# Optimization experiments

Hardware: AMD Instinct MI355X
Metric: run time of the kernel (lower is better)

## Reference

```python
import jax, jax.numpy as jnp
import numpy as np

N = 65536      # tokens
D = 512        # input_dim
H = 8          # num_heads
HD = 64        # head_dim
FF = 2048      # hidden_dim
EPS = 1e-5


def _layer_norm(x, g, b):
    mu = jnp.mean(x, axis=-1, keepdims=True)
    var = jnp.mean(jnp.square(x - mu), axis=-1, keepdims=True)
    return (x - mu) * jax.lax.rsqrt(var + EPS) * g + b


def setup_inputs() -> dict:
    key = jax.random.key(0)
    ks = jax.random.split(key, 12)
    s_d = 1.0 / np.sqrt(D)
    s_f = 1.0 / np.sqrt(FF)
    return {
        "x":   jax.random.normal(ks[0], (N, D), jnp.float32),
        # Linear weights stored [in, out] (transpose of torch's [out, in])
        "Wq":  jax.random.uniform(ks[1], (D, D), jnp.float32, -s_d, s_d),
        "bq":  jnp.zeros((D,), jnp.float32),
        "Wk":  jax.random.uniform(ks[2], (D, D), jnp.float32, -s_d, s_d),
        "bk":  jnp.zeros((D,), jnp.float32),
        "Wv":  jax.random.uniform(ks[3], (D, D), jnp.float32, -s_d, s_d),
        "bv":  jnp.zeros((D,), jnp.float32),
        "ln1_g": jnp.ones((D,), jnp.float32),
        "ln1_b": jnp.zeros((D,), jnp.float32),
        "W1":  jax.random.uniform(ks[4], (D, FF), jnp.float32, -s_d, s_d),
        "b1":  jnp.zeros((FF,), jnp.float32),
        "W2":  jax.random.uniform(ks[5], (FF, D), jnp.float32, -s_f, s_f),
        "b2":  jnp.zeros((D,), jnp.float32),
        "ln2_g": jnp.ones((D,), jnp.float32),
        "ln2_b": jnp.zeros((D,), jnp.float32),
    }


def reference(x, Wq, bq, Wk, bk, Wv, bv, ln1_g, ln1_b, W1, b1, W2, b2, ln2_g, ln2_b):
    n = x.shape[0]
    # --- multi-head attention (per-token head mixing, as in source) ---
    q = (x @ Wq + bq).reshape(n, H, HD)
    k = (x @ Wk + bk).reshape(n, H, HD)
    v = (x @ Wv + bv).reshape(n, H, HD)
    # score[n] = q[n] @ k[n]^T : [H, H] per token
    score = jnp.einsum("nhd,ngd->nhg", q, k) / jnp.sqrt(jnp.float32(HD))
    attn = jax.nn.softmax(score, axis=-1)
    ctx = jnp.einsum("nhg,ngd->nhd", attn, v).reshape(n, D)
    y = _layer_norm(x + ctx, ln1_g, ln1_b)
    # --- feed forward with residual + layer norm ---
    h = jax.nn.relu(y @ W1 + b1)
    z = h @ W2 + b2 + y
    return _layer_norm(z, ln2_g, ln2_b)
```

## Files before the change

### kernel.cpp

```cpp
#include <hip/hip_runtime.h>
#include <cstdint>


typedef __attribute__((ext_vector_type(8))) short bf16x8;
typedef __attribute__((ext_vector_type(4))) float f32x4;
typedef __attribute__((ext_vector_type(8))) unsigned short u16x8;

__device__ __forceinline__ float bf2f(unsigned short u) {
  union { unsigned int i; float f; } v; v.i = ((unsigned int)u) << 16; return v.f;
}
__device__ __forceinline__ unsigned short f2bf(float f) {
  union { float f; unsigned int i; } v; v.f = f;
  unsigned int r = v.i + 0x7FFFu + ((v.i >> 16) & 1u);
  return (unsigned short)(r >> 16);
}

#define GLD16(g, l)                                                         \
  __builtin_amdgcn_global_load_lds(                                         \
      (const __attribute__((address_space(1))) void*)(g),                   \
      (__attribute__((address_space(3))) void*)(l), 16, 0, 0)

__global__ __launch_bounds__(256) void cast_f32_bf16(
    const float* __restrict__ in, ushort* __restrict__ out) {
  const size_t i = (size_t)blockIdx.x * 256 + threadIdx.x;
  const float4* p = (const float4*)in + i * 2;
  float4 a = p[0], b = p[1];
  u16x8 r;
  r[0] = f2bf(a.x); r[1] = f2bf(a.y); r[2] = f2bf(a.z); r[3] = f2bf(a.w);
  r[4] = f2bf(b.x); r[5] = f2bf(b.y); r[6] = f2bf(b.z); r[7] = f2bf(b.w);
  ((u16x8*)out)[i] = r;
}

__global__ __launch_bounds__(256) void transpose_cast(
    const float* __restrict__ W, ushort* __restrict__ Wt,
    int K, int Nn, int rowoff, int ldt) {
  __shared__ float tile[32][33];
  const int tx = threadIdx.x & 31, ty = threadIdx.x >> 5;
  const int nb = blockIdx.x * 32, kb = blockIdx.y * 32;
#pragma unroll
  for (int s = 0; s < 4; ++s)
    tile[ty + 8 * s][tx] = W[(size_t)(kb + ty + 8 * s) * Nn + nb + tx];
  __syncthreads();
#pragma unroll
  for (int s = 0; s < 4; ++s)
    Wt[(size_t)(rowoff + nb + ty + 8 * s) * ldt + kb + tx] =
        f2bf(tile[tx][ty + 8 * s]);
}

template <int EPI>
__global__ __launch_bounds__(512, 2) void gemm_bt(
    const ushort* __restrict__ A, const ushort* __restrict__ Bt,
    int N, int K, void* __restrict__ Cout,
    const float* __restrict__ bias0, const float* __restrict__ bias1,
    const float* __restrict__ bias2, const ushort* __restrict__ resid) {
  constexpr int BK = 32;
  __shared__ __align__(16) ushort lds[4 * 16384];
  const int tid = threadIdx.x;
  const int wid = tid >> 6, lane = tid & 63;
  const int wm = wid >> 2, wn = wid & 3;

  const int gx = gridDim.x;
  const int nwg = gx * gridDim.y;
  const int orig = blockIdx.y * gx + blockIdx.x;
  const int q8 = nwg >> 3, r8 = nwg & 7;
  const int xcd = orig & 7, loc = orig >> 3;
  const int swz = (xcd < r8) ? (xcd * (q8 + 1) + loc)
                             : (r8 * (q8 + 1) + (xcd - r8) * q8 + loc);
  const size_t m0 = (size_t)(swz / gx) * 256;
  const size_t n0 = (size_t)(swz % gx) * 256;
  const int NT = K / BK;

  const int sgcol = (((tid & 3) - ((tid >> 3) & 3)) & 3) << 3;
  const ushort* a0 = A + (m0 + (tid >> 2)) * (size_t)K + sgcol;
  const ushort* b0 = Bt + (n0 + (tid >> 2)) * (size_t)K + sgcol;
  const size_t rowK = 128 * (size_t)K;
  ushort* ldst = &lds[tid * 8];

#define STAGE_SLOT(t, sl)                                                   \
  {                                                                         \
    ushort* d = ldst + ((t) & 3) * 16384 + (sl) * 4096;                     \
    const ushort* g = (((sl) < 2) ? a0 : b0) + (size_t)(t) * BK +           \
                      (((sl) & 1) ? rowK : 0);                              \
    GLD16(g, d);                                                            \
  }

  const int cswz = ((((lane >> 4) + ((lane >> 1) & 3)) & 3) << 3);
  const int arow = wm * 128 + (lane & 15);
  const int brow = wn * 64 + (lane & 15);

  f32x4 acc[8][4] = {};

#pragma unroll
  for (int pt = 0; pt < 3; ++pt) {
    STAGE_SLOT(pt, 0); STAGE_SLOT(pt, 1);
    STAGE_SLOT(pt, 2); STAGE_SLOT(pt, 3);
  }

  for (int t = 0; t < NT; ++t) {
    if (t < NT - 2) {
      asm volatile("s_waitcnt vmcnt(8)" ::: "memory");
    } else if (t == NT - 2) {
      asm volatile("s_waitcnt vmcnt(4)" ::: "memory");
    } else {
      asm volatile("s_waitcnt vmcnt(0)" ::: "memory");
    }
    __builtin_amdgcn_s_barrier();

    const ushort* lA = &lds[(t & 3) * 16384];
    const ushort* lB = lA + 8192;

    if (t + 3 < NT) {
      STAGE_SLOT(t + 3, 0); STAGE_SLOT(t + 3, 1);
      STAGE_SLOT(t + 3, 2); STAGE_SLOT(t + 3, 3);
    }

    bf16x8 bfr[4], af[8];
#pragma unroll
    for (int ni = 0; ni < 4; ++ni)
      bfr[ni] = *(const bf16x8*)&lB[(brow + ni * 16) * 32 + cswz];
#pragma unroll
    for (int mi = 0; mi < 8; ++mi)
      af[mi] = *(const bf16x8*)&lA[(arow + mi * 16) * 32 + cswz];

    __builtin_amdgcn_s_setprio(1);
#pragma unroll
    for (int mi = 0; mi < 8; ++mi)
#pragma unroll
      for (int ni = 0; ni < 4; ++ni)
        acc[mi][ni] = __builtin_amdgcn_mfma_f32_16x16x32_bf16(
            af[mi], bfr[ni], acc[mi][ni], 0, 0, 0);
    __builtin_amdgcn_s_setprio(0);
  }
#undef STAGE_SLOT

  const int lm = lane & 15, lq = lane >> 4;
  size_t col[4];
  float bv[4];
#pragma unroll
  for (int ni = 0; ni < 4; ++ni) {
    col[ni] = n0 + wn * 64 + ni * 16 + lm;
    if (EPI == 0) {
      const float* bp = (n0 < 512) ? bias0 : ((n0 < 1024) ? bias1 : bias2);
      bv[ni] = bp[col[ni] & 511];
    } else {
      bv[ni] = bias0[col[ni]];
    }
  }
#pragma unroll
  for (int mi = 0; mi < 8; ++mi) {
#pragma unroll
    for (int j = 0; j < 4; ++j) {
      const size_t row = m0 + wm * 128 + mi * 16 + lq * 4 + j;
#pragma unroll
      for (int ni = 0; ni < 4; ++ni) {
        float v = acc[mi][ni][j] + bv[ni];
        if (EPI == 0) {
          ((ushort*)Cout)[row * N + col[ni]] = f2bf(v);
        } else if (EPI == 1) {
          ((ushort*)Cout)[row * N + col[ni]] = f2bf(fmaxf(v, 0.f));
        } else {
          v += bf2f(resid[row * N + col[ni]]);
          ((ushort*)Cout)[row * N + col[ni]] = f2bf(v);
        }
      }
    }
  }
}

__global__ __launch_bounds__(256) void attn_ln1(
    const ushort* __restrict__ qkv, const ushort* __restrict__ xb,
    const float* __restrict__ g1, const float* __restrict__ b1,
    ushort* __restrict__ y) {
  const int lane = threadIdx.x & 63;
  const size_t t = (size_t)blockIdx.x * 4 + (threadIdx.x >> 6);
  const ushort* base = qkv + t * 1536;
  float qd[8], kd[8], vd[8];
#pragma unroll
  for (int h = 0; h < 8; ++h) {
    qd[h] = bf2f(base[h * 64 + lane]);
    kd[h] = bf2f(base[512 + h * 64 + lane]);
    vd[h] = bf2f(base[1024 + h * 64 + lane]);
  }

  const bool lb0 = lane & 1, lb1 = lane & 2, lb2 = lane & 4;
  const bool lb3 = lane & 8, lb4 = lane & 16, lb5 = lane & 32;

  float c1[32];
#pragma unroll
  for (int f = 0; f < 32; ++f) {
    const int i0 = 2 * f, i1 = 2 * f + 1;
    const float a0 = qd[i0 >> 3] * kd[i0 & 7];
    const float a1 = qd[i1 >> 3] * kd[i1 & 7];
    const float keep = lb0 ? a1 : a0;
    const float send = lb0 ? a0 : a1;
    c1[f] = keep + __shfl_xor(send, 1, 64);
  }
  float c2[16];
#pragma unroll
  for (int f = 0; f < 16; ++f) {
    const float keep = lb1 ? c1[2 * f + 1] : c1[2 * f];
    const float send = lb1 ? c1[2 * f] : c1[2 * f + 1];
    c2[f] = keep + __shfl_xor(send, 2, 64);
  }
  float c3[8];
#pragma unroll
  for (int f = 0; f < 8; ++f) {
    const float keep = lb2 ? c2[2 * f + 1] : c2[2 * f];
    const float send = lb2 ? c2[2 * f] : c2[2 * f + 1];
    c3[f] = keep + __shfl_xor(send, 4, 64);
  }
  float c4[4];
#pragma unroll
  for (int f = 0; f < 4; ++f) {
    const float keep = lb3 ? c3[2 * f + 1] : c3[2 * f];
    const float send = lb3 ? c3[2 * f] : c3[2 * f + 1];
    c4[f] = keep + __shfl_xor(send, 8, 64);
  }
  float c5[2];
#pragma unroll
  for (int f = 0; f < 2; ++f) {
    const float keep = lb4 ? c4[2 * f + 1] : c4[2 * f];
    const float send = lb4 ? c4[2 * f] : c4[2 * f + 1];
    c5[f] = keep + __shfl_xor(send, 16, 64);
  }
  const float keep = lb5 ? c5[1] : c5[0];
  const float send = lb5 ? c5[0] : c5[1];
  const float s = keep + __shfl_xor(send, 32, 64);

  float mx = s;
  mx = fmaxf(mx, __shfl_xor(mx, 1, 64));
  mx = fmaxf(mx, __shfl_xor(mx, 2, 64));
  mx = fmaxf(mx, __shfl_xor(mx, 4, 64));
  const float e = __expf((s - mx) * 0.125f);
  float sum = e;
  sum += __shfl_xor(sum, 1, 64);
  sum += __shfl_xor(sum, 2, 64);
  sum += __shfl_xor(sum, 4, 64);
  const float a = e * __builtin_amdgcn_rcpf(sum);

  const int ai = __float_as_int(a);
  float r[8];
#pragma unroll
  for (int h = 0; h < 8; ++h) {
    float c = 0.f;
#pragma unroll
    for (int g = 0; g < 8; ++g) {
      const float w = __int_as_float(__builtin_amdgcn_readlane(ai, h * 8 + g));
      c = fmaf(w, vd[g], c);
    }
    r[h] = bf2f(xb[t * 512 + h * 64 + lane]) + c;
  }

  float sm = 0.f, sq = 0.f;
#pragma unroll
  for (int h = 0; h < 8; ++h) { sm += r[h]; sq += r[h] * r[h]; }
#pragma unroll
  for (int m = 1; m < 64; m <<= 1) {
    sm += __shfl_xor(sm, m, 64);
    sq += __shfl_xor(sq, m, 64);
  }
  const float mu = sm * (1.f / 512.f);
  const float var = sq * (1.f / 512.f) - mu * mu;
  const float rs = rsqrtf(var + 1e-5f);
#pragma unroll
  for (int h = 0; h < 8; ++h) {
    const int d = h * 64 + lane;
    y[t * 512 + d] = f2bf((r[h] - mu) * rs * g1[d] + b1[d]);
  }
}

__global__ __launch_bounds__(256) void ln_out(
    const ushort* __restrict__ zb, const float* __restrict__ g2,
    const float* __restrict__ b2, float* __restrict__ out) {
  const int lane = threadIdx.x & 63;
  const size_t t = (size_t)blockIdx.x * 4 + (threadIdx.x >> 6);
  const u16x8 v = ((const u16x8*)(zb + t * 512))[lane];
  float r[8];
  float sm = 0.f, sq = 0.f;
#pragma unroll
  for (int j = 0; j < 8; ++j) {
    r[j] = bf2f(v[j]);
    sm += r[j];
    sq += r[j] * r[j];
  }
#pragma unroll
  for (int m = 1; m < 64; m <<= 1) {
    sm += __shfl_xor(sm, m, 64);
    sq += __shfl_xor(sq, m, 64);
  }
  const float mu = sm * (1.f / 512.f);
  const float rs = rsqrtf(sq * (1.f / 512.f) - mu * mu + 1e-5f);
  const int d0 = lane * 8;
  const float4 ga = *(const float4*)(g2 + d0);
  const float4 gb = *(const float4*)(g2 + d0 + 4);
  const float4 ba = *(const float4*)(b2 + d0);
  const float4 bb = *(const float4*)(b2 + d0 + 4);
  float4 oa, ob;
  oa.x = (r[0] - mu) * rs * ga.x + ba.x;
  oa.y = (r[1] - mu) * rs * ga.y + ba.y;
  oa.z = (r[2] - mu) * rs * ga.z + ba.z;
  oa.w = (r[3] - mu) * rs * ga.w + ba.w;
  ob.x = (r[4] - mu) * rs * gb.x + bb.x;
  ob.y = (r[5] - mu) * rs * gb.y + bb.y;
  ob.z = (r[6] - mu) * rs * gb.z + bb.z;
  ob.w = (r[7] - mu) * rs * gb.w + bb.w;
  float* o = out + t * 512 + d0;
  *(float4*)o = oa;
  *(float4*)(o + 4) = ob;
}

extern "C" void kernel_launch(void* const* d_in, const int* in_sizes, int n_in,
                              void* d_out, int out_size, void* d_ws,
                              size_t ws_size, hipStream_t stream) {
  const float* x    = (const float*)d_in[0];
  const float* Wq   = (const float*)d_in[1];
  const float* bq   = (const float*)d_in[2];
  const float* Wk   = (const float*)d_in[3];
  const float* bk   = (const float*)d_in[4];
  const float* Wv   = (const float*)d_in[5];
  const float* bv   = (const float*)d_in[6];
  const float* ln1g = (const float*)d_in[7];
  const float* ln1b = (const float*)d_in[8];
  const float* W1   = (const float*)d_in[9];
  const float* b1   = (const float*)d_in[10];
  const float* W2   = (const float*)d_in[11];
  const float* b2   = (const float*)d_in[12];
  const float* ln2g = (const float*)d_in[13];
  const float* ln2b = (const float*)d_in[14];
  float* out = (float*)d_out;

  const int Ntok = in_sizes[0] / 512;

  char* ws = (char*)d_ws;
  ushort* Wqkvt = (ushort*)ws;
  ushort* W1t   = Wqkvt + (size_t)1536 * 512;
  ushort* W2t   = W1t + (size_t)2048 * 512;
  const size_t woff = ((size_t)1536 * 512 + (size_t)2048 * 512 +
                       (size_t)512 * 2048) * 2;

  size_t avail = (ws_size > woff) ? (ws_size - woff) : 0;
  long long Cll = (long long)(avail / 9216);
  Cll = (Cll / 256) * 256;
  if (Cll > 32768) Cll = 32768;
  if (Cll > Ntok) Cll = Ntok;
  if (Cll < 256) Cll = 256;
  const int C = (int)Cll;

  char* cb = ws + woff;
  ushort* xb  = (ushort*)cb;
  ushort* y   = xb + (size_t)C * 512;
  ushort* qkv = y + (size_t)C * 512;
  ushort* hb  = qkv + (size_t)C * 1536;
  ushort* zb  = qkv;

  transpose_cast<<<dim3(16, 16), dim3(256), 0, stream>>>(Wq, Wqkvt, 512, 512, 0, 512);
  transpose_cast<<<dim3(16, 16), dim3(256), 0, stream>>>(Wk, Wqkvt, 512, 512, 512, 512);
  transpose_cast<<<dim3(16, 16), dim3(256), 0, stream>>>(Wv, Wqkvt, 512, 512, 1024, 512);
  transpose_cast<<<dim3(64, 16), dim3(256), 0, stream>>>(W1, W1t, 512, 2048, 0, 512);
  transpose_cast<<<dim3(16, 64), dim3(256), 0, stream>>>(W2, W2t, 2048, 512, 0, 2048);

  for (int t0 = 0; t0 < Ntok; t0 += C) {
    const int Cc = (Ntok - t0 < C) ? (Ntok - t0) : C;
    const float* xc = x + (size_t)t0 * 512;

    cast_f32_bf16<<<dim3((Cc * 512) / 2048), dim3(256), 0, stream>>>(xc, xb);

    gemm_bt<0><<<dim3(1536 / 256, Cc / 256), dim3(512), 0, stream>>>(
        xb, Wqkvt, 1536, 512, qkv, bq, bk, bv, nullptr);

    attn_ln1<<<dim3(Cc / 4), dim3(256), 0, stream>>>(qkv, xb, ln1g, ln1b, y);

    gemm_bt<1><<<dim3(2048 / 256, Cc / 256), dim3(512), 0, stream>>>(
        y, W1t, 2048, 512, hb, b1, nullptr, nullptr, nullptr);

    gemm_bt<2><<<dim3(512 / 256, Cc / 256), dim3(512), 0, stream>>>(
        hb, W2t, 512, 2048, zb, b2, nullptr, nullptr, y);

    ln_out<<<dim3(Cc / 4), dim3(256), 0, stream>>>(
        zb, ln2g, ln2b, out + (size_t)t0 * 512);
  }
}
```

Baseline: 637.1 us.

## Restructure GEMM mainloop into BK=64 double-buffered, four-phase interleaved schedule

```diff
diff --git a/kernel.cpp b/kernel.cpp
--- a/kernel.cpp
+++ b/kernel.cpp
@@ -48,16 +48,17 @@
 }
 
 template <int EPI>
-__global__ __launch_bounds__(512, 2) void gemm_bt(
+__global__ __launch_bounds__(512, 1) void gemm_bt(
     const ushort* __restrict__ A, const ushort* __restrict__ Bt,
     int N, int K, void* __restrict__ Cout,
     const float* __restrict__ bias0, const float* __restrict__ bias1,
     const float* __restrict__ bias2, const ushort* __restrict__ resid) {
-  constexpr int BK = 32;
-  __shared__ __align__(16) ushort lds[4 * 16384];
+  __shared__ __align__(16) ushort lds[2 * 32768];
   const int tid = threadIdx.x;
   const int wid = tid >> 6, lane = tid & 63;
   const int wm = wid >> 2, wn = wid & 3;
+  const int li = lane & 15, q = lane >> 4;
+  const int sw = (lane >> 1) & 7;
 
   const int gx = gridDim.x;
   const int nwg = gx * gridDim.y;
@@ -68,77 +69,136 @@
                              : (r8 * (q8 + 1) + (xcd - r8) * q8 + loc);
   const size_t m0 = (size_t)(swz / gx) * 256;
   const size_t n0 = (size_t)(swz % gx) * 256;
-  const int NT = K / BK;
-
-  const int sgcol = (((tid & 3) - ((tid >> 3) & 3)) & 3) << 3;
-  const ushort* a0 = A + (m0 + (tid >> 2)) * (size_t)K + sgcol;
-  const ushort* b0 = Bt + (n0 + (tid >> 2)) * (size_t)K + sgcol;
-  const size_t rowK = 128 * (size_t)K;
-  ushort* ldst = &lds[tid * 8];
-
-#define STAGE_SLOT(t, sl)                                                   \
+  const int NT = K >> 6;
+
+  const int ssrc = (((tid & 7) - ((tid >> 4) & 7)) & 7) << 3;
+  const ushort* asrc = A + (m0 + (tid >> 3)) * (size_t)K + ssrc;
+  const ushort* bsrc = Bt + (n0 + (tid >> 3)) * (size_t)K + ssrc;
+  const size_t rowK64 = 64 * (size_t)K;
+  const size_t rowK128 = 128 * (size_t)K;
+
+#define STAGE_HALF(v, arr, h)                                               \
   {                                                                         \
-    ushort* d = ldst + ((t) & 3) * 16384 + (sl) * 4096;                     \
-    const ushort* g = (((sl) < 2) ? a0 : b0) + (size_t)(t) * BK +           \
-                      (((sl) & 1) ? rowK : 0);                              \
-    GLD16(g, d);                                                            \
-  }
-
-  const int cswz = ((((lane >> 4) + ((lane >> 1) & 3)) & 3) << 3);
-  const int arow = wm * 128 + (lane & 15);
-  const int brow = wn * 64 + (lane & 15);
+    ushort* dst =                                                           \
+        &lds[((v) & 1) * 32768 + (arr) * 16384 + (h) * 8192 + tid * 8];     \
+    const ushort* g = ((arr) ? bsrc : asrc) + (size_t)(v) * 64 +            \
+                      ((h) ? rowK128 : 0);                                  \
+    GLD16(g, dst);                                                          \
+    GLD16(g + rowK64, dst + 4096);                                          \
+  }
+
+  const int arow = wm * 128 + li;
+  const int brow = wn * 64 + li;
+#define RD_A(mi, ks)                                                        \
+  (*(const bf16x8*)&dA[(arow + (mi) * 16) * 64 +                            \
+                       ((((ks) * 4 + q + sw) & 7) << 3)])
+#define RD_B(ni, ks)                                                        \
+  (*(const bf16x8*)&dB[(brow + (ni) * 16) * 64 +                            \
+                       ((((ks) * 4 + q + sw) & 7) << 3)])
 
   f32x4 acc[8][4] = {};
 
-#pragma unroll
-  for (int pt = 0; pt < 3; ++pt) {
-    STAGE_SLOT(pt, 0); STAGE_SLOT(pt, 1);
-    STAGE_SLOT(pt, 2); STAGE_SLOT(pt, 3);
-  }
+  STAGE_HALF(0, 0, 0); STAGE_HALF(0, 0, 1);
+  STAGE_HALF(0, 1, 0); STAGE_HALF(0, 1, 1);
+  if (NT > 1) { STAGE_HALF(1, 1, 0); STAGE_HALF(1, 1, 1); }
 
   for (int t = 0; t < NT; ++t) {
-    if (t < NT - 2) {
-      asm volatile("s_waitcnt vmcnt(8)" ::: "memory");
-    } else if (t == NT - 2) {
+    if (t < NT - 1) {
       asm volatile("s_waitcnt vmcnt(4)" ::: "memory");
     } else {
       asm volatile("s_waitcnt vmcnt(0)" ::: "memory");
     }
     __builtin_amdgcn_s_barrier();
 
-    const ushort* lA = &lds[(t & 3) * 16384];
-    const ushort* lB = lA + 8192;
-
-    if (t + 3 < NT) {
-      STAGE_SLOT(t + 3, 0); STAGE_SLOT(t + 3, 1);
-      STAGE_SLOT(t + 3, 2); STAGE_SLOT(t + 3, 3);
-    }
-
-    bf16x8 bfr[4], af[8];
-#pragma unroll
-    for (int ni = 0; ni < 4; ++ni)
-      bfr[ni] = *(const bf16x8*)&lB[(brow + ni * 16) * 32 + cswz];
-#pragma unroll
-    for (int mi = 0; mi < 8; ++mi)
-      af[mi] = *(const bf16x8*)&lA[(arow + mi * 16) * 32 + cswz];
-
+    const ushort* dA = &lds[(t & 1) * 32768];
+    const ushort* dB = dA + 16384;
+    bf16x8 a_[4][2], b01[2][2], b23[2][2];
+
+#pragma unroll
+    for (int mi = 0; mi < 4; ++mi) {
+      a_[mi][0] = RD_A(mi, 0); a_[mi][1] = RD_A(mi, 1);
+    }
+#pragma unroll
+    for (int ni = 0; ni < 2; ++ni) {
+      b01[ni][0] = RD_B(ni, 0); b01[ni][1] = RD_B(ni, 1);
+    }
+    if (t + 1 < NT) STAGE_HALF(t + 1, 0, 0);
+    __builtin_amdgcn_s_barrier();
     __builtin_amdgcn_s_setprio(1);
 #pragma unroll
-    for (int mi = 0; mi < 8; ++mi)
-#pragma unroll
-      for (int ni = 0; ni < 4; ++ni)
+    for (int mi = 0; mi < 4; ++mi)
+#pragma unroll
+      for (int ni = 0; ni < 2; ++ni) {
         acc[mi][ni] = __builtin_amdgcn_mfma_f32_16x16x32_bf16(
-            af[mi], bfr[ni], acc[mi][ni], 0, 0, 0);
+            a_[mi][0], b01[ni][0], acc[mi][ni], 0, 0, 0);
+        acc[mi][ni] = __builtin_amdgcn_mfma_f32_16x16x32_bf16(
+            a_[mi][1], b01[ni][1], acc[mi][ni], 0, 0, 0);
+      }
     __builtin_amdgcn_s_setprio(0);
-  }
-#undef STAGE_SLOT
-
-  const int lm = lane & 15, lq = lane >> 4;
+    __builtin_amdgcn_s_barrier();
+
+#pragma unroll
+    for (int ni = 0; ni < 2; ++ni) {
+      b23[ni][0] = RD_B(ni + 2, 0); b23[ni][1] = RD_B(ni + 2, 1);
+    }
+    if (t + 1 < NT) STAGE_HALF(t + 1, 0, 1);
+    __builtin_amdgcn_s_barrier();
+    __builtin_amdgcn_s_setprio(1);
+#pragma unroll
+    for (int mi = 0; mi < 4; ++mi)
+#pragma unroll
+      for (int ni = 0; ni < 2; ++ni) {
+        acc[mi][ni + 2] = __builtin_amdgcn_mfma_f32_16x16x32_bf16(
+            a_[mi][0], b23[ni][0], acc[mi][ni + 2], 0, 0, 0);
+        acc[mi][ni + 2] = __builtin_amdgcn_mfma_f32_16x16x32_bf16(
+            a_[mi][1], b23[ni][1], acc[mi][ni + 2], 0, 0, 0);
+      }
+    __builtin_amdgcn_s_setprio(0);
+    __builtin_amdgcn_s_barrier();
+
+#pragma unroll
+    for (int mi = 0; mi < 4; ++mi) {
+      a_[mi][0] = RD_A(mi + 4, 0); a_[mi][1] = RD_A(mi + 4, 1);
+    }
+    if (t + 2 < NT) STAGE_HALF(t + 2, 1, 0);
+    __builtin_amdgcn_s_barrier();
+    __builtin_amdgcn_s_setprio(1);
+#pragma unroll
+    for (int mi = 0; mi < 4; ++mi)
+#pragma unroll
+      for (int ni = 0; ni < 2; ++ni) {
+        acc[mi + 4][ni + 2] = __builtin_amdgcn_mfma_f32_16x16x32_bf16(
+            a_[mi][0], b23[ni][0], acc[mi + 4][ni + 2], 0, 0, 0);
+        acc[mi + 4][ni + 2] = __builtin_amdgcn_mfma_f32_16x16x32_bf16(
+            a_[mi][1], b23[ni][1], acc[mi + 4][ni + 2], 0, 0, 0);
+      }
+    __builtin_amdgcn_s_setprio(0);
+    __builtin_amdgcn_s_barrier();
+
+    if (t + 2 < NT) STAGE_HALF(t + 2, 1, 1);
+    __builtin_amdgcn_s_barrier();
+    __builtin_amdgcn_s_setprio(1);
+#pragma unroll
+    for (int mi = 0; mi < 4; ++mi)
+#pragma unroll
+      for (int ni = 0; ni < 2; ++ni) {
+        acc[mi + 4][ni] = __builtin_amdgcn_mfma_f32_16x16x32_bf16(
+            a_[mi][0], b01[ni][0], acc[mi + 4][ni], 0, 0, 0);
+        acc[mi + 4][ni] = __builtin_amdgcn_mfma_f32_16x16x32_bf16(
+            a_[mi][1], b01[ni][1], acc[mi + 4][ni], 0, 0, 0);
+      }
+    __builtin_amdgcn_s_setprio(0);
+    __builtin_amdgcn_s_barrier();
+  }
+#undef STAGE_HALF
+#undef RD_A
+#undef RD_B
+
   size_t col[4];
   float bv[4];
 #pragma unroll
   for (int ni = 0; ni < 4; ++ni) {
-    col[ni] = n0 + wn * 64 + ni * 16 + lm;
+    col[ni] = n0 + wn * 64 + ni * 16 + li;
     if (EPI == 0) {
       const float* bp = (n0 < 512) ? bias0 : ((n0 < 1024) ? bias1 : bias2);
       bv[ni] = bp[col[ni] & 511];
@@ -150,7 +210,7 @@
   for (int mi = 0; mi < 8; ++mi) {
 #pragma unroll
     for (int j = 0; j < 4; ++j) {
-      const size_t row = m0 + wm * 128 + mi * 16 + lq * 4 + j;
+      const size_t row = m0 + wm * 128 + mi * 16 + q * 4 + j;
 #pragma unroll
       for (int ni = 0; ni < 4; ++ni) {
         float v = acc[mi][ni][j] + bv[ni];
```

After: 631.7 us. About the same (-0.8%).
